# Optimization experiments

Measured on AMD Instinct MI355X. Metric: run time of the kernel, lower is better.

The kernel has to match this reference:

```python
import jax, jax.numpy as jnp
import numpy as np

NUM_NODES = 100000
IN_CH = 128
OUT_CH = 64
NUM_EDGES = 1000000


def setup_inputs() -> dict:
    key = jax.random.key(0)
    ks = jax.random.split(key, 16)

    x = jax.random.normal(ks[0], (NUM_NODES, IN_CH), dtype=jnp.float32)

    def make_edges(k_src, k_tgt, k_w):
        src = jax.random.randint(k_src, (NUM_EDGES,), 0, NUM_NODES, dtype=jnp.int32)
        # tf.math.segment_sum requires sorted segment ids -> sort targets
        tgt = jnp.sort(jax.random.randint(k_tgt, (NUM_EDGES,), 0, NUM_NODES, dtype=jnp.int32))
        ei = jnp.stack([src, tgt], axis=0)  # (2, E)
        ew = jax.random.uniform(k_w, (NUM_EDGES,), dtype=jnp.float32)
        return ei, ew

    edge_index_in, edge_weight_in = make_edges(ks[1], ks[2], ks[3])
    edge_index_out, edge_weight_out = make_edges(ks[4], ks[5], ks[6])

    glorot = (6.0 / (IN_CH + OUT_CH)) ** 0.5
    W_main_in = jax.random.uniform(ks[7], (IN_CH, OUT_CH), minval=-glorot, maxval=glorot, dtype=jnp.float32)
    W_main_out = jax.random.uniform(ks[8], (IN_CH, OUT_CH), minval=-glorot, maxval=glorot, dtype=jnp.float32)
    W_shared = jax.random.uniform(ks[9], (IN_CH, OUT_CH), minval=-glorot, maxval=glorot, dtype=jnp.float32)

    bias_main_in = jnp.zeros((OUT_CH,), dtype=jnp.float32)
    bias_main_out = jnp.zeros((OUT_CH,), dtype=jnp.float32)
    bias_shared_in = jnp.zeros((OUT_CH,), dtype=jnp.float32)
    bias_shared_out = jnp.zeros((OUT_CH,), dtype=jnp.float32)

    C_in_vec = jnp.ones((NUM_NODES, 1), dtype=jnp.float32)
    C_out_vec = jnp.ones((NUM_NODES, 1), dtype=jnp.float32)

    return {
        "x": x,
        "W_main_in": W_main_in,
        "W_main_out": W_main_out,
        "W_shared": W_shared,
        "bias_main_in": bias_main_in,
        "bias_main_out": bias_main_out,
        "bias_shared_in": bias_shared_in,
        "bias_shared_out": bias_shared_out,
        "C_in_vec": C_in_vec,
        "C_out_vec": C_out_vec,
        "edge_index_in": edge_index_in,
        "edge_weight_in": edge_weight_in,
        "edge_index_out": edge_index_out,
        "edge_weight_out": edge_weight_out,
    }


def _propagate(h, edge_index, edge_weight, num_nodes):
    # gather messages from source nodes, scale by edge weight, sum into targets
    src = edge_index[0]
    tgt = edge_index[1]
    msgs = h[src] * edge_weight[:, None]  # (E, OUT_CH)
    return jax.ops.segment_sum(msgs, tgt, num_segments=num_nodes)  # (N, OUT_CH)


def reference(x, W_main_in, W_main_out, W_shared,
              bias_main_in, bias_main_out, bias_shared_in, bias_shared_out,
              C_in_vec, C_out_vec,
              edge_index_in, edge_weight_in, edge_index_out, edge_weight_out):
    n = x.shape[0]
    h_main_in = _propagate(x @ W_main_in, edge_index_in, edge_weight_in, n)
    h_shared_in = _propagate(x @ W_shared, edge_index_in, edge_weight_in, n)
    ic_combined = h_main_in + bias_main_in + (h_shared_in + bias_shared_in)

    h_main_out = _propagate(x @ W_main_out, edge_index_out, edge_weight_out, n)
    h_shared_out = _propagate(x @ W_shared, edge_index_out, edge_weight_out, n)
    oc_combined = h_main_out + bias_main_out + (h_shared_out + bias_shared_out)

    return C_in_vec * ic_combined + C_out_vec * oc_combined
```

## Files before the change

kernel.cpp:

```cpp
#include <hip/hip_runtime.h>

#define IN_CH   128
#define OUT_CH  64
#define M_TILE  128
#define XS_PITCH 136

typedef __attribute__((ext_vector_type(8))) short short8;
typedef __attribute__((ext_vector_type(4))) float floatx4;

__device__ __forceinline__ unsigned short f2bf(float f) {
    union { float f; unsigned u; } v; v.f = f;
    unsigned r = v.u + 0x7fffu + ((v.u >> 16) & 1u);
    return (unsigned short)(r >> 16);
}
__device__ __forceinline__ float bfl(unsigned u) {
    return __uint_as_float(u << 16);
}
__device__ __forceinline__ float bfh(unsigned u) {
    return __uint_as_float(u & 0xffff0000u);
}

__global__ void prep_kernel(const int* __restrict__ tgtIn,
                            const int* __restrict__ tgtOut,
                            const float* __restrict__ Wmi,
                            const float* __restrict__ Wmo,
                            const float* __restrict__ Wsh,
                            int* __restrict__ rpIn,
                            int* __restrict__ rpOut,
                            unsigned short* __restrict__ WcT,
                            int n_nodes, int neIn, int neOut)
{
    int i = blockIdx.x * blockDim.x + threadIdx.x;
    const int nIn1 = neIn + 1, nOut1 = neOut + 1;

    if (i < nIn1 + nOut1) {
        const int* tgt; int* rp; int idx; int ne;
        if (i < nIn1) { tgt = tgtIn;  rp = rpIn;  idx = i;        ne = neIn; }
        else          { tgt = tgtOut; rp = rpOut; idx = i - nIn1; ne = neOut; }
        if (idx < ne) {
            int a    = tgt[idx];
            int prev = (idx == 0) ? -1 : tgt[idx - 1];
            for (int t = prev + 1; t <= a; ++t) rp[t] = idx;
        } else {
            int last = (ne > 0) ? tgt[ne - 1] : -1;
            for (int t = last + 1; t <= n_nodes; ++t) rp[t] = ne;
        }
    } else {
        int j = i - (nIn1 + nOut1);
        if (j < 2 * OUT_CH * IN_CH) {
            int n = j >> 7, k = j & 127;
            float m = (n < OUT_CH) ? Wmi[k * OUT_CH + n]
                                   : Wmo[k * OUT_CH + (n - OUT_CH)];
            float s = Wsh[k * OUT_CH + (n & (OUT_CH - 1))];
            WcT[n * IN_CH + k] = f2bf(m + s);
        }
    }
}

__global__ __launch_bounds__(256, 3)
void gemm_kernel(const float* __restrict__ x,
                 const unsigned short* __restrict__ WcT,
                 unsigned short* __restrict__ Abf,
                 unsigned short* __restrict__ Bbf,
                 int n_nodes)
{
    __shared__ unsigned short Xs[M_TILE][XS_PITCH];

    const int tid  = threadIdx.x;
    const int w    = tid >> 6;
    const int lane = tid & 63;
    const int l15  = lane & 15;
    const int quad = lane >> 4;
    const long long node0 = (long long)blockIdx.x * M_TILE;

    short8 bfrag[4][2];
#pragma unroll
    for (int ks = 0; ks < 4; ++ks)
#pragma unroll
        for (int ni = 0; ni < 2; ++ni)
            bfrag[ks][ni] = *(const short8*)&WcT[(w * 32 + ni * 16 + l15) * IN_CH
                                                 + ks * 32 + quad * 8];

    {
        const float4* x4 = (const float4*)x;
        for (int i = tid; i < M_TILE * (IN_CH / 4); i += 256) {
            int row = i >> 5, c4 = i & 31;
            long long node = node0 + row;
            float4 v = make_float4(0.f, 0.f, 0.f, 0.f);
            if (node < n_nodes) v = x4[node * (IN_CH / 4) + c4];
            uint2 p;
            p.x = ((unsigned)f2bf(v.y) << 16) | f2bf(v.x);
            p.y = ((unsigned)f2bf(v.w) << 16) | f2bf(v.z);
            *(uint2*)&Xs[row][c4 * 4] = p;
        }
    }
    __syncthreads();

    floatx4 acc[8][2];
#pragma unroll
    for (int mi = 0; mi < 8; ++mi)
#pragma unroll
        for (int ni = 0; ni < 2; ++ni)
            acc[mi][ni] = (floatx4){0.f, 0.f, 0.f, 0.f};

#pragma unroll
    for (int ks = 0; ks < 4; ++ks) {
        const int k0 = ks * 32 + quad * 8;
#pragma unroll
        for (int mi = 0; mi < 8; ++mi) {
            short8 a = *(const short8*)&Xs[mi * 16 + l15][k0];
            acc[mi][0] = __builtin_amdgcn_mfma_f32_16x16x32_bf16(a, bfrag[ks][0], acc[mi][0], 0, 0, 0);
            acc[mi][1] = __builtin_amdgcn_mfma_f32_16x16x32_bf16(a, bfrag[ks][1], acc[mi][1], 0, 0, 0);
        }
    }

    __syncthreads();
    const int colb = w * 32;
#pragma unroll
    for (int mi = 0; mi < 8; ++mi)
#pragma unroll
        for (int ni = 0; ni < 2; ++ni)
#pragma unroll
            for (int r = 0; r < 4; ++r)
                Xs[mi * 16 + quad * 4 + r][colb + ni * 16 + l15] =
                    f2bf(acc[mi][ni][r]);
    __syncthreads();

    for (int i = tid; i < M_TILE * 16; i += 256) {
        int row  = i >> 4;
        int half = (i >> 3) & 1;
        int v4   = i & 7;
        long long node = node0 + row;
        if (node < n_nodes) {
            uint4 v = *(const uint4*)&Xs[row][half * 64 + v4 * 8];
            unsigned short* dst = half ? Bbf : Abf;
            *(uint4*)&dst[node * OUT_CH + v4 * 8] = v;
        }
    }
}

__global__ __launch_bounds__(256)
void prop_kernel(const unsigned short* __restrict__ H,
                 const int* __restrict__ rpIn, const int* __restrict__ rpOut,
                 const int* __restrict__ srcIn, const float* __restrict__ ewIn,
                 const int* __restrict__ srcOut, const float* __restrict__ ewOut,
                 const float* __restrict__ bmi, const float* __restrict__ bmo,
                 const float* __restrict__ bsi, const float* __restrict__ bso,
                 const float* __restrict__ Cin, const float* __restrict__ Cout,
                 float* __restrict__ out, int n_nodes, int neIn, int neOut)
{
    const int lane = threadIdx.x & 63;
    const int wv   = threadIdx.x >> 6;
    const int e    = lane >> 3;
    const int el   = lane & 7;
    const int ch8  = el * 8;
    const int eb   = lane & 56;

    const unsigned short* Hq = H + ch8;

    const int t = ((int)blockIdx.x * 4 + wv) * 8 + e;
    const bool valid = (t < n_nodes);
    const int tc = valid ? t : 0;

    const int Boff = n_nodes * OUT_CH;

    int ei0 = rpIn[tc],  ei1 = rpIn[tc + 1];
    int eo0 = rpOut[tc], eo1 = rpOut[tc + 1];
    int dIn  = ei1 - ei0;
    int len  = valid ? (dIn + (eo1 - eo0)) : 0;
    float ci = Cin[tc], co = Cout[tc];

    int ml = len;
    ml = max(ml, __shfl_xor(ml, 8));
    ml = max(ml, __shfl_xor(ml, 16));
    ml = max(ml, __shfl_xor(ml, 32));
    const int maxlen = __builtin_amdgcn_readfirstlane(ml);

    float a0 = 0.f, a1 = 0.f, a2 = 0.f, a3 = 0.f;
    float a4 = 0.f, a5 = 0.f, a6 = 0.f, a7 = 0.f;

    auto load_raw = [&](int j, int& sI, float& wI, int& sO, float& wO) {
        int iIn  = min(ei0 + max(0, min(j, dIn - 1)), neIn - 1);
        int jo   = j - dIn;
        int iOut = min(eo0 + max(0, jo), neOut - 1);
        sI = srcIn[iIn];  wI = ewIn[iIn];
        sO = srcOut[iOut]; wO = ewOut[iOut];
    };

    auto conv = [&](int p, int sI, float wI, int sO, float wO,
                    int& rowb, float& wj) {
        int j = p + el;
        bool inSeg  = (j < dIn);
        bool anySeg = (j < len);
        int rb = inSeg ? (sI * OUT_CH) : (sO * OUT_CH + Boff);
        rowb = anySeg ? rb : 0;
        wj   = inSeg ? (ci * wI) : (anySeg ? (co * wO) : 0.f);
    };

    auto gather = [&](int rowb, uint4 (&u)[8]) {
        int r0 = __shfl(rowb, eb + 0), r1 = __shfl(rowb, eb + 1);
        int r2 = __shfl(rowb, eb + 2), r3 = __shfl(rowb, eb + 3);
        int r4 = __shfl(rowb, eb + 4), r5 = __shfl(rowb, eb + 5);
        int r6 = __shfl(rowb, eb + 6), r7 = __shfl(rowb, eb + 7);
        u[0] = *(const uint4*)(Hq + r0);
        u[1] = *(const uint4*)(Hq + r1);
        u[2] = *(const uint4*)(Hq + r2);
        u[3] = *(const uint4*)(Hq + r3);
        u[4] = *(const uint4*)(Hq + r4);
        u[5] = *(const uint4*)(Hq + r5);
        u[6] = *(const uint4*)(Hq + r6);
        u[7] = *(const uint4*)(Hq + r7);
    };

    auto consume = [&](const uint4 (&u)[8], float wj) {
#pragma unroll
        for (int k = 0; k < 8; ++k) {
            float wk = __shfl(wj, eb + k);
            uint4 uk = u[k];
            a0 += wk * bfl(uk.x); a1 += wk * bfh(uk.x);
            a2 += wk * bfl(uk.y); a3 += wk * bfh(uk.y);
            a4 += wk * bfl(uk.z); a5 += wk * bfh(uk.z);
            a6 += wk * bfl(uk.w); a7 += wk * bfh(uk.w);
        }
    };

    int   sIa, sOa, sIb, sOb;
    float wIa, wOa, wIb, wOb;
    uint4 uA[8], uB[8];
    float wjA = 0.f, wjB = 0.f;

    load_raw(el,     sIa, wIa, sOa, wOa);
    load_raw(8 + el, sIb, wIb, sOb, wOb);
    {
        int rb; conv(0, sIa, wIa, sOa, wOa, rb, wjA);
        gather(rb, uA);
    }
    load_raw(16 + el, sIa, wIa, sOa, wOa);
    {
        int rb; conv(8, sIb, wIb, sOb, wOb, rb, wjB);
        gather(rb, uB);
    }
    load_raw(24 + el, sIb, wIb, sOb, wOb);

    for (int p = 0; p < maxlen; p += 16) {
        consume(uA, wjA);
        if (p + 16 < maxlen) {
            int rb; conv(p + 16, sIa, wIa, sOa, wOa, rb, wjA);
            load_raw(p + 32 + el, sIa, wIa, sOa, wOa);
            gather(rb, uA);
        }
        if (p + 8 < maxlen) consume(uB, wjB);
        if (p + 24 < maxlen) {
            int rb; conv(p + 24, sIb, wIb, sOb, wOb, rb, wjB);
            load_raw(p + 40 + el, sIb, wIb, sOb, wOb);
            gather(rb, uB);
        }
    }

    if (valid) {
        float4 o0, o1;
        o0.x = a0 + ci * (bmi[ch8 + 0] + bsi[ch8 + 0]) + co * (bmo[ch8 + 0] + bso[ch8 + 0]);
        o0.y = a1 + ci * (bmi[ch8 + 1] + bsi[ch8 + 1]) + co * (bmo[ch8 + 1] + bso[ch8 + 1]);
        o0.z = a2 + ci * (bmi[ch8 + 2] + bsi[ch8 + 2]) + co * (bmo[ch8 + 2] + bso[ch8 + 2]);
        o0.w = a3 + ci * (bmi[ch8 + 3] + bsi[ch8 + 3]) + co * (bmo[ch8 + 3] + bso[ch8 + 3]);
        o1.x = a4 + ci * (bmi[ch8 + 4] + bsi[ch8 + 4]) + co * (bmo[ch8 + 4] + bso[ch8 + 4]);
        o1.y = a5 + ci * (bmi[ch8 + 5] + bsi[ch8 + 5]) + co * (bmo[ch8 + 5] + bso[ch8 + 5]);
        o1.z = a6 + ci * (bmi[ch8 + 6] + bsi[ch8 + 6]) + co * (bmo[ch8 + 6] + bso[ch8 + 6]);
        o1.w = a7 + ci * (bmi[ch8 + 7] + bsi[ch8 + 7]) + co * (bmo[ch8 + 7] + bso[ch8 + 7]);
        float* ob = out + (long long)t * OUT_CH + ch8;
        *(float4*)ob = o0;
        *(float4*)(ob + 4) = o1;
    }
}

extern "C" void kernel_launch(void* const* d_in, const int* in_sizes, int n_in,
                              void* d_out, int out_size, void* d_ws, size_t ws_size,
                              hipStream_t stream)
{
    const float* x    = (const float*)d_in[0];
    const float* Wmi  = (const float*)d_in[1];
    const float* Wmo  = (const float*)d_in[2];
    const float* Wsh  = (const float*)d_in[3];
    const float* bmi  = (const float*)d_in[4];
    const float* bmo  = (const float*)d_in[5];
    const float* bsi  = (const float*)d_in[6];
    const float* bso  = (const float*)d_in[7];
    const float* Cin  = (const float*)d_in[8];
    const float* Cout = (const float*)d_in[9];
    const int*   eiIn  = (const int*)d_in[10];
    const float* ewIn  = (const float*)d_in[11];
    const int*   eiOut = (const int*)d_in[12];
    const float* ewOut = (const float*)d_in[13];

    const int n_nodes = in_sizes[0] / IN_CH;
    const int neIn  = in_sizes[11];
    const int neOut = in_sizes[13];

    const int* srcIn  = eiIn;
    const int* tgtIn  = eiIn + neIn;
    const int* srcOut = eiOut;
    const int* tgtOut = eiOut + neOut;

    char* ws = (char*)d_ws;
    size_t NH = (size_t)n_nodes * OUT_CH * sizeof(unsigned short);
    unsigned short* Abf = (unsigned short*)ws;
    unsigned short* Bbf = (unsigned short*)(ws + NH);
    int* rpIn  = (int*)(ws + 2 * NH);
    int* rpOut = rpIn + (n_nodes + 1);
    unsigned short* WcT = (unsigned short*)(rpOut + (n_nodes + 1));

    int prep_threads = (neIn + 1) + (neOut + 1) + 2 * OUT_CH * IN_CH;
    prep_kernel<<<(prep_threads + 255) / 256, 256, 0, stream>>>(
        tgtIn, tgtOut, Wmi, Wmo, Wsh, rpIn, rpOut, WcT, n_nodes, neIn, neOut);

    int gblocks = (n_nodes + M_TILE - 1) / M_TILE;
    gemm_kernel<<<gblocks, 256, 0, stream>>>(x, WcT, Abf, Bbf, n_nodes);

    int pblocks = (n_nodes + 31) / 32;
    prop_kernel<<<pblocks, 256, 0, stream>>>(
        Abf, rpIn, rpOut, srcIn, ewIn, srcOut, ewOut,
        bmi, bmo, bsi, bso, Cin, Cout, (float*)d_out, n_nodes, neIn, neOut);
}
```

Before: 182.3 us.

## Fuse prep work into GEMM kernel and shrink propagation blocks to one wave

Removes the separate prep kernel. Its row-pointer construction moves into the GEMM kernel as a grid-stride loop, and each GEMM block now combines and converts the weights to bf16 itself, straight into its MFMA fragments. This saves one kernel launch and the WcT round trip through memory. In exchange every block does redundant strided weight reads and the rowptr writes. The propagation kernel now launches 64-thread blocks instead of 256, which changes scheduling granularity.

```diff
diff --git a/kernel.cpp b/kernel.cpp
--- a/kernel.cpp
+++ b/kernel.cpp
@@ -20,53 +20,42 @@
     return __uint_as_float(u & 0xffff0000u);
 }
 
-__global__ void prep_kernel(const int* __restrict__ tgtIn,
-                            const int* __restrict__ tgtOut,
-                            const float* __restrict__ Wmi,
-                            const float* __restrict__ Wmo,
-                            const float* __restrict__ Wsh,
-                            int* __restrict__ rpIn,
-                            int* __restrict__ rpOut,
-                            unsigned short* __restrict__ WcT,
-                            int n_nodes, int neIn, int neOut)
-{
-    int i = blockIdx.x * blockDim.x + threadIdx.x;
-    const int nIn1 = neIn + 1, nOut1 = neOut + 1;
-
-    if (i < nIn1 + nOut1) {
-        const int* tgt; int* rp; int idx; int ne;
-        if (i < nIn1) { tgt = tgtIn;  rp = rpIn;  idx = i;        ne = neIn; }
-        else          { tgt = tgtOut; rp = rpOut; idx = i - nIn1; ne = neOut; }
-        if (idx < ne) {
-            int a    = tgt[idx];
-            int prev = (idx == 0) ? -1 : tgt[idx - 1];
-            for (int t = prev + 1; t <= a; ++t) rp[t] = idx;
-        } else {
-            int last = (ne > 0) ? tgt[ne - 1] : -1;
-            for (int t = last + 1; t <= n_nodes; ++t) rp[t] = ne;
-        }
-    } else {
-        int j = i - (nIn1 + nOut1);
-        if (j < 2 * OUT_CH * IN_CH) {
-            int n = j >> 7, k = j & 127;
-            float m = (n < OUT_CH) ? Wmi[k * OUT_CH + n]
-                                   : Wmo[k * OUT_CH + (n - OUT_CH)];
-            float s = Wsh[k * OUT_CH + (n & (OUT_CH - 1))];
-            WcT[n * IN_CH + k] = f2bf(m + s);
-        }
-    }
-}
-
 __global__ __launch_bounds__(256, 3)
 void gemm_kernel(const float* __restrict__ x,
-                 const unsigned short* __restrict__ WcT,
+                 const float* __restrict__ Wmi,
+                 const float* __restrict__ Wmo,
+                 const float* __restrict__ Wsh,
+                 const int* __restrict__ tgtIn,
+                 const int* __restrict__ tgtOut,
+                 int* __restrict__ rpIn,
+                 int* __restrict__ rpOut,
                  unsigned short* __restrict__ Abf,
                  unsigned short* __restrict__ Bbf,
-                 int n_nodes)
+                 int n_nodes, int neIn, int neOut)
 {
     __shared__ unsigned short Xs[M_TILE][XS_PITCH];
 
     const int tid  = threadIdx.x;
+
+    {
+        const int nIn1 = neIn + 1, nOut1 = neOut + 1;
+        const int total = nIn1 + nOut1;
+        const int stride = gridDim.x * 256;
+        for (int i = (int)blockIdx.x * 256 + tid; i < total; i += stride) {
+            const int* tgt; int* rp; int idx; int ne;
+            if (i < nIn1) { tgt = tgtIn;  rp = rpIn;  idx = i;        ne = neIn; }
+            else          { tgt = tgtOut; rp = rpOut; idx = i - nIn1; ne = neOut; }
+            if (idx < ne) {
+                int a    = tgt[idx];
+                int prev = (idx == 0) ? -1 : tgt[idx - 1];
+                for (int t = prev + 1; t <= a; ++t) rp[t] = idx;
+            } else {
+                int last = (ne > 0) ? tgt[ne - 1] : -1;
+                for (int t = last + 1; t <= n_nodes; ++t) rp[t] = ne;
+            }
+        }
+    }
+
     const int w    = tid >> 6;
     const int lane = tid & 63;
     const int l15  = lane & 15;
@@ -77,9 +66,18 @@
 #pragma unroll
     for (int ks = 0; ks < 4; ++ks)
 #pragma unroll
-        for (int ni = 0; ni < 2; ++ni)
-            bfrag[ks][ni] = *(const short8*)&WcT[(w * 32 + ni * 16 + l15) * IN_CH
-                                                 + ks * 32 + quad * 8];
+        for (int ni = 0; ni < 2; ++ni) {
+            const int n_col = w * 32 + ni * 16 + l15;
+            const float* Wm = (n_col < OUT_CH) ? Wmi : Wmo;
+            const int nn = n_col & (OUT_CH - 1);
+            short8 bf;
+#pragma unroll
+            for (int j = 0; j < 8; ++j) {
+                int k = ks * 32 + quad * 8 + j;
+                bf[j] = (short)f2bf(Wm[k * OUT_CH + nn] + Wsh[k * OUT_CH + nn]);
+            }
+            bfrag[ks][ni] = bf;
+        }
 
     {
         const float4* x4 = (const float4*)x;
@@ -139,7 +137,7 @@
     }
 }
 
-__global__ __launch_bounds__(256)
+__global__ __launch_bounds__(64)
 void prop_kernel(const unsigned short* __restrict__ H,
                  const int* __restrict__ rpIn, const int* __restrict__ rpOut,
                  const int* __restrict__ srcIn, const float* __restrict__ ewIn,
@@ -150,7 +148,6 @@
                  float* __restrict__ out, int n_nodes, int neIn, int neOut)
 {
     const int lane = threadIdx.x & 63;
-    const int wv   = threadIdx.x >> 6;
     const int e    = lane >> 3;
     const int el   = lane & 7;
     const int ch8  = el * 8;
@@ -158,7 +155,7 @@
 
     const unsigned short* Hq = H + ch8;
 
-    const int t = ((int)blockIdx.x * 4 + wv) * 8 + e;
+    const int t = (int)blockIdx.x * 8 + e;
     const bool valid = (t < n_nodes);
     const int tc = valid ? t : 0;
 
@@ -307,17 +304,14 @@
     unsigned short* Bbf = (unsigned short*)(ws + NH);
     int* rpIn  = (int*)(ws + 2 * NH);
     int* rpOut = rpIn + (n_nodes + 1);
-    unsigned short* WcT = (unsigned short*)(rpOut + (n_nodes + 1));
-
-    int prep_threads = (neIn + 1) + (neOut + 1) + 2 * OUT_CH * IN_CH;
-    prep_kernel<<<(prep_threads + 255) / 256, 256, 0, stream>>>(
-        tgtIn, tgtOut, Wmi, Wmo, Wsh, rpIn, rpOut, WcT, n_nodes, neIn, neOut);
 
     int gblocks = (n_nodes + M_TILE - 1) / M_TILE;
-    gemm_kernel<<<gblocks, 256, 0, stream>>>(x, WcT, Abf, Bbf, n_nodes);
-
-    int pblocks = (n_nodes + 31) / 32;
-    prop_kernel<<<pblocks, 256, 0, stream>>>(
+    gemm_kernel<<<gblocks, 256, 0, stream>>>(
+        x, Wmi, Wmo, Wsh, tgtIn, tgtOut, rpIn, rpOut, Abf, Bbf,
+        n_nodes, neIn, neOut);
+
+    int pblocks = (n_nodes + 7) / 8;
+    prop_kernel<<<pblocks, 64, 0, stream>>>(
         Abf, rpIn, rpOut, srcIn, ewIn, srcOut, ewOut,
         bmi, bmo, bsi, bso, Cin, Cout, (float*)d_out, n_nodes, neIn, neOut);
 }
```

Result: slower. 193.7 us (+6.2%).
